# Optimization experiments

Measured on AMD Instinct MI355X. Metric: run time of the kernel, lower is better.

Reference implementation:

```python
import jax, jax.numpy as jnp
import numpy as np

DT = 0.01          # discretization timestep (init kwarg dt)
DAMP_MIN = 5e-4    # minimum damping (init kwarg damp_min)
BATCH, SEQ, D_IN, N_STATE = 16, 2048, 1024, 128


def setup_inputs() -> dict:
    key = jax.random.key(0)
    k1, k2, k3, k4, k5 = jax.random.split(key, 5)
    u = jax.random.normal(k1, (BATCH, SEQ, D_IN), jnp.float32)
    # A_real init: randn*0.1 - damp_min, then clamped to <= -damp_min (stability)
    A_real = jnp.minimum(jax.random.normal(k2, (N_STATE,), jnp.float32) * 0.1 - DAMP_MIN, -DAMP_MIN)
    A_imag = jax.random.normal(k3, (N_STATE,), jnp.float32)
    B = jax.random.normal(k4, (N_STATE, D_IN), jnp.float32) * 0.02
    C = jax.random.normal(k5, (D_IN, N_STATE), jnp.float32) * 0.02
    return {"u": u, "A_real": A_real, "A_imag": A_imag, "B": B, "C": C}


def reference(u, A_real, A_imag, B, C):
    """Real-input path of StableResonantSSM.

    Bilinear discretization of diagonal complex A:
      a_disc = (1 + dt/2 * a) / (1 - dt/2 * a)          (elementwise, A diagonal)
      B_disc = sqrt(dt) * B / (1 - dt/2 * a)            (row-wise scaling)
    Recurrence: h_t = a_disc * h_{t-1} + B_disc @ u_t;  y_t = Re(C @ h_t).
    """
    dt = jnp.float32(DT)
    a = (A_real + 1j * A_imag).astype(jnp.complex64)          # (N,)
    denom = 1.0 - (dt / 2) * a                                 # (N,) complex
    a_disc = (1.0 + (dt / 2) * a) / denom                      # (N,)
    B_disc = (jnp.sqrt(dt) * B.astype(jnp.complex64)) / denom[:, None]  # (N, D)

    # Precompute all input injections as one GEMM: (T, B, N) complex
    Bu = jnp.einsum('btd,nd->tbn', u, B_disc)

    def step(h, bu_t):
        h = a_disc * h + bu_t
        return h, h

    h0 = jnp.zeros((u.shape[0], a.shape[0]), jnp.complex64)
    _, hs = jax.lax.scan(step, h0, Bu)                         # hs: (T, B, N)

    # C is real, so Re(C @ h) == C @ Re(h)
    y = jnp.einsum('tbn,dn->btd', hs.real, C)                  # (B, T, D)
    return y
```

## Files before the change

### kernel.cpp

```cpp
#include <hip/hip_runtime.h>
#include <hip/hip_bf16.h>
#include <cstdint>

#define DT_F    0.01f
#define NB      16
#define T_SEQ   2048
#define DD      1024
#define NS      128
#define CHUNK   64
#define NCH     32

using f32x4  = __attribute__((ext_vector_type(4))) float;
using bf16x8 = __attribute__((ext_vector_type(8))) short;
using fl4    = __attribute__((ext_vector_type(4))) float;

#define AS1(p) ((const __attribute__((address_space(1))) void*)(p))
#define AS3(p) ((__attribute__((address_space(3))) void*)(p))

__device__ __forceinline__ unsigned short f2bf(float f) {
  union { float f; unsigned u; } v; v.f = f;
  unsigned r = v.u + 0x7fffu + ((v.u >> 16) & 1u);
  return (unsigned short)(r >> 16);
}
__device__ __forceinline__ float bf2f(unsigned short s) {
  union { unsigned u; float f; } v; v.u = ((unsigned)s) << 16;
  return v.f;
}
__device__ __forceinline__ unsigned short f2bf_hw(float f) {
  __hip_bfloat16 h = __float2bfloat16(f);
  return __builtin_bit_cast(unsigned short, h);
}

__global__ void prep_all(const float* __restrict__ Ar, const float* __restrict__ Ai,
                         const float* __restrict__ B, const float* __restrict__ C,
                         unsigned short* __restrict__ W, unsigned short* __restrict__ Cb,
                         float* __restrict__ ad) {
  const int blk = blockIdx.x;
  const int tid = threadIdx.x;
  if (blk < 512) {
    const int i = blk * 256 + tid;
    Cb[i] = f2bf(C[i]);
    return;
  }
  const int n = blk - 512;
  const float ar = Ar[n], ai = Ai[n];
  const float dr = 1.f - 0.5f * DT_F * ar;
  const float di = -0.5f * DT_F * ai;
  const float inv = 1.f / (dr * dr + di * di);
  const float nr = 1.f + 0.5f * DT_F * ar;
  const float ni = 0.5f * DT_F * ai;
  if (tid == 0) {
    ad[n]      = (nr * dr + ni * di) * inv;
    ad[NS + n] = (ni * dr - nr * di) * inv;
  }
  const float s  = sqrtf(DT_F);
  const float cr = s * dr * inv;
  const float ci = -s * di * inv;
  for (int d = tid; d < DD; d += 256) {
    const float b = B[(size_t)n * DD + d];
    W[(size_t)n * DD + d]        = f2bf(b * cr);
    W[(size_t)(NS + n) * DD + d] = f2bf(b * ci);
  }
}

__global__ __launch_bounds__(256) void gemm1(const float* __restrict__ U,
                                             const unsigned short* __restrict__ Bw,
                                             unsigned short* __restrict__ Bu) {
  __shared__ __align__(16) unsigned short As[128 * 64];
  __shared__ __align__(16) unsigned short Bs[128 * 64];
  const int tid  = threadIdx.x;
  const int lane = tid & 63;
  const int wave = tid >> 6;

  const int L   = blockIdx.x;
  const int xcd = L & 7;
  const int k   = L >> 3;
  const int bm  = xcd * 32 + (k >> 1);
  const int bn  = k & 1;
  const int rowA0 = bm * 128, colB0 = bn * 128;
  const int wm = (wave >> 1) * 64, wn = (wave & 1) * 64;

  f32x4 acc[4][4];
  const f32x4 zero = {0.f, 0.f, 0.f, 0.f};
#pragma unroll
  for (int i = 0; i < 4; ++i)
#pragma unroll
    for (int j = 0; j < 4; ++j) acc[i][j] = zero;

  const int srow = tid >> 3;
  const int scol = (tid & 7) * 8;
  const int grow = wave * 8 + (lane >> 3);
  const int gcol = (lane & 7) * 8;

  for (int k0 = 0; k0 < DD; k0 += 64) {
    __syncthreads();
#pragma unroll
    for (int it = 0; it < 4; ++it) {
      const unsigned short* gb = Bw + (size_t)(colB0 + it * 32 + grow) * DD + k0 + gcol;
      __builtin_amdgcn_global_load_lds(AS1(gb), AS3(&Bs[(it * 32 + wave * 8) * 64]), 16, 0, 0);
    }
#pragma unroll
    for (int it = 0; it < 4; ++it) {
      const int r = it * 32 + srow;
      const float* ga = U + (size_t)(rowA0 + r) * DD + k0 + scol;
      fl4 v0 = *(const fl4*)ga;
      fl4 v1 = *(const fl4*)(ga + 4);
      bf16x8 pk;
#pragma unroll
      for (int e = 0; e < 4; ++e) { pk[e] = (short)f2bf_hw(v0[e]); pk[4 + e] = (short)f2bf_hw(v1[e]); }
      *(bf16x8*)&As[r * 64 + scol] = pk;
    }
    __syncthreads();
#pragma unroll
    for (int ks = 0; ks < 2; ++ks) {
      bf16x8 af[4], bfr[4];
#pragma unroll
      for (int i = 0; i < 4; ++i)
        af[i] = *(const bf16x8*)&As[(wm + i * 16 + (lane & 15)) * 64 + ks * 32 + (lane >> 4) * 8];
#pragma unroll
      for (int j = 0; j < 4; ++j)
        bfr[j] = *(const bf16x8*)&Bs[(wn + j * 16 + (lane & 15)) * 64 + ks * 32 + (lane >> 4) * 8];
#pragma unroll
      for (int i = 0; i < 4; ++i)
#pragma unroll
        for (int j = 0; j < 4; ++j)
          acc[i][j] = __builtin_amdgcn_mfma_f32_16x16x32_bf16(af[i], bfr[j], acc[i][j], 0, 0, 0);
    }
  }

#pragma unroll
  for (int i = 0; i < 4; ++i) {
    const int r0 = rowA0 + wm + i * 16 + (lane >> 4) * 4;
#pragma unroll
    for (int j = 0; j < 4; ++j) {
      const int c = colB0 + wn + j * 16 + (lane & 15);
#pragma unroll
      for (int q = 0; q < 4; ++q)
        Bu[(size_t)(r0 + q) * 256 + c] = f2bf_hw(acc[i][j][q]);
    }
  }
}

__global__ void scan_finals(const unsigned short* __restrict__ Bu,
                            const float* __restrict__ ad, float* __restrict__ F) {
  const int c = blockIdx.x, b = blockIdx.y;
  const int n = threadIdx.x;
  const float ar = ad[n], ai = ad[NS + n];
  float hr = 0.f, hi = 0.f;
  const unsigned short* p = Bu + ((size_t)b * T_SEQ + (size_t)c * CHUNK) * 256;
#pragma unroll 8
  for (int t = 0; t < CHUNK; ++t) {
    const float br = bf2f(p[t * 256 + n]);
    const float bi = bf2f(p[t * 256 + 128 + n]);
    const float nr = fmaf(ar, hr, fmaf(-ai, hi, br));
    const float ni = fmaf(ar, hi, fmaf(ai, hr, bi));
    hr = nr; hi = ni;
  }
  F[((size_t)b * NCH + c) * 256 + n]       = hr;
  F[((size_t)b * NCH + c) * 256 + 128 + n] = hi;
}

__global__ __launch_bounds__(256) void gemm2s(const unsigned short* __restrict__ Bu,
                                              const float* __restrict__ F,
                                              const float* __restrict__ ad,
                                              const unsigned short* __restrict__ Cb,
                                              float* __restrict__ y) {
  __shared__ __align__(16) unsigned short Hl[64 * 128];
  const int tid  = threadIdx.x;
  const int lane = tid & 63;
  const int wave = tid >> 6;
  const int L = blockIdx.x;
  const int b = L >> 5;
  const int c = L & 31;

  if (tid < 128) {
    const int n = tid;
    const float ar = ad[n], ai = ad[NS + n];
    float alr = ar, ali = ai;
#pragma unroll
    for (int s = 0; s < 6; ++s) {
      const float tr = alr * alr - ali * ali;
      const float ti = 2.f * alr * ali;
      alr = tr; ali = ti;
    }
    float hr = 0.f, hi = 0.f;
    for (int cc = 0; cc < c; ++cc) {
      const float fr = F[((size_t)b * NCH + cc) * 256 + n];
      const float fi = F[((size_t)b * NCH + cc) * 256 + 128 + n];
      const float nr = fmaf(alr, hr, fmaf(-ali, hi, fr));
      const float ni = fmaf(alr, hi, fmaf(ali, hr, fi));
      hr = nr; hi = ni;
    }
    const unsigned short* p = Bu + ((size_t)b * T_SEQ + (size_t)c * CHUNK) * 256;
#pragma unroll 8
    for (int t = 0; t < CHUNK; ++t) {
      const float br = bf2f(p[t * 256 + n]);
      const float bi = bf2f(p[t * 256 + 128 + n]);
      const float nr = fmaf(ar, hr, fmaf(-ai, hi, br));
      const float ni = fmaf(ar, hi, fmaf(ai, hr, bi));
      hr = nr; hi = ni;
      const int byte = t * 256 + ((n * 2) ^ ((t & 7) << 4));
      *(unsigned short*)((char*)Hl + byte) = f2bf(hr);
    }
  }
  __syncthreads();

  const size_t row0 = (size_t)b * T_SEQ + (size_t)c * CHUNK;
#pragma unroll
  for (int cg = 0; cg < 4; ++cg) {
    const int d0 = wave * 256 + cg * 64;
    f32x4 acc[4][4];
    const f32x4 zero = {0.f, 0.f, 0.f, 0.f};
#pragma unroll
    for (int i = 0; i < 4; ++i)
#pragma unroll
      for (int j = 0; j < 4; ++j) acc[i][j] = zero;

#pragma unroll
    for (int ks = 0; ks < 4; ++ks) {
      bf16x8 af[4], bfr[4];
#pragma unroll
      for (int i = 0; i < 4; ++i) {
        const int r = i * 16 + (lane & 15);
        const int byte = r * 256 + ((ks * 64 + (lane >> 4) * 16) ^ ((r & 7) << 4));
        af[i] = *(const bf16x8*)((const char*)Hl + byte);
      }
#pragma unroll
      for (int j = 0; j < 4; ++j) {
        const unsigned short* gb = Cb + (size_t)(d0 + j * 16 + (lane & 15)) * NS + ks * 32 + (lane >> 4) * 8;
        bfr[j] = *(const bf16x8*)gb;
      }
#pragma unroll
      for (int i = 0; i < 4; ++i)
#pragma unroll
        for (int j = 0; j < 4; ++j)
          acc[i][j] = __builtin_amdgcn_mfma_f32_16x16x32_bf16(af[i], bfr[j], acc[i][j], 0, 0, 0);
    }

#pragma unroll
    for (int i = 0; i < 4; ++i) {
      const size_t r0 = row0 + i * 16 + (lane >> 4) * 4;
#pragma unroll
      for (int j = 0; j < 4; ++j) {
        const int d = d0 + j * 16 + (lane & 15);
#pragma unroll
        for (int q = 0; q < 4; ++q)
          y[(r0 + q) * DD + d] = acc[i][j][q];
      }
    }
  }
}

extern "C" void kernel_launch(void* const* d_in, const int* in_sizes, int n_in,
                              void* d_out, int out_size, void* d_ws, size_t ws_size,
                              hipStream_t stream) {
  const float* u  = (const float*)d_in[0];
  const float* Ar = (const float*)d_in[1];
  const float* Ai = (const float*)d_in[2];
  const float* B  = (const float*)d_in[3];
  const float* C  = (const float*)d_in[4];
  float* y = (float*)d_out;
  char* ws = (char*)d_ws;

  unsigned short* W  = (unsigned short*)(ws);
  unsigned short* Cb = (unsigned short*)(ws + (512 << 10));
  float*          ad = (float*)(ws + (768 << 10));
  unsigned short* Bu = (unsigned short*)(ws + (1 << 20));
  float*          F  = (float*)(ws + (1 << 20) + 16777216);

  prep_all<<<dim3(640), dim3(256), 0, stream>>>(Ar, Ai, B, C, W, Cb, ad);
  gemm1<<<dim3(512), dim3(256), 0, stream>>>(u, W, Bu);
  scan_finals<<<dim3(NCH, NB), dim3(128), 0, stream>>>(Bu, ad, F);
  gemm2s<<<dim3(NB * NCH), dim3(256), 0, stream>>>(Bu, F, ad, Cb, y);
}
```

Measured before the change: 89.91 us.

## Fuse input GEMM with chunk-local scan and apply carry correction in output GEMM

The input-projection GEMM now tiles one 64-step chunk by all 256 complex state columns per block, so each block can run the chunk-local scan from LDS right after the MFMA loop. It writes the local states (bf16) and chunk finals, which removes the separate scan_finals kernel and the re-read of Bu. The output kernel loads the local states via global_load_lds, then adds the propagated carry (a^(t+1) times the incoming state) instead of rescanning the chunk. In exchange, the B operand is reloaded per 64-row block, the carry term adds an extra bf16 rounding, and occupancy depends on 40KB of LDS.

```diff
diff --git a/kernel.cpp b/kernel.cpp
--- a/kernel.cpp
+++ b/kernel.cpp
@@ -31,10 +31,19 @@
   return __builtin_bit_cast(unsigned short, h);
 }
 
+__device__ __forceinline__ void adisc(float Arn, float Ain, float& ar, float& ai) {
+  const float dr = 1.f - 0.5f * DT_F * Arn;
+  const float di = -0.5f * DT_F * Ain;
+  const float inv = 1.f / (dr * dr + di * di);
+  const float nr = 1.f + 0.5f * DT_F * Arn;
+  const float nim = 0.5f * DT_F * Ain;
+  ar = (nr * dr + nim * di) * inv;
+  ai = (nim * dr - nr * di) * inv;
+}
+
 __global__ void prep_all(const float* __restrict__ Ar, const float* __restrict__ Ai,
                          const float* __restrict__ B, const float* __restrict__ C,
-                         unsigned short* __restrict__ W, unsigned short* __restrict__ Cb,
-                         float* __restrict__ ad) {
+                         unsigned short* __restrict__ W, unsigned short* __restrict__ Cb) {
   const int blk = blockIdx.x;
   const int tid = threadIdx.x;
   if (blk < 512) {
@@ -47,12 +56,6 @@
   const float dr = 1.f - 0.5f * DT_F * ar;
   const float di = -0.5f * DT_F * ai;
   const float inv = 1.f / (dr * dr + di * di);
-  const float nr = 1.f + 0.5f * DT_F * ar;
-  const float ni = 0.5f * DT_F * ai;
-  if (tid == 0) {
-    ad[n]      = (nr * dr + ni * di) * inv;
-    ad[NS + n] = (ni * dr - nr * di) * inv;
-  }
   const float s  = sqrtf(DT_F);
   const float cr = s * dr * inv;
   const float ci = -s * di * inv;
@@ -63,22 +66,22 @@
   }
 }
 
-__global__ __launch_bounds__(256) void gemm1(const float* __restrict__ U,
-                                             const unsigned short* __restrict__ Bw,
-                                             unsigned short* __restrict__ Bu) {
-  __shared__ __align__(16) unsigned short As[128 * 64];
-  __shared__ __align__(16) unsigned short Bs[128 * 64];
+__global__ __launch_bounds__(256, 2) void gemm1s(const float* __restrict__ U,
+                                                 const float* __restrict__ Ar,
+                                                 const float* __restrict__ Ai,
+                                                 const unsigned short* __restrict__ W,
+                                                 unsigned short* __restrict__ Hs,
+                                                 float* __restrict__ F) {
+  __shared__ __align__(16) char smem[40960];
+  unsigned short* As = (unsigned short*)smem;
+  unsigned short* Bs = (unsigned short*)(smem + 8192);
+  char*           Bt = smem;
+
   const int tid  = threadIdx.x;
   const int lane = tid & 63;
   const int wave = tid >> 6;
-
-  const int L   = blockIdx.x;
-  const int xcd = L & 7;
-  const int k   = L >> 3;
-  const int bm  = xcd * 32 + (k >> 1);
-  const int bn  = k & 1;
-  const int rowA0 = bm * 128, colB0 = bn * 128;
-  const int wm = (wave >> 1) * 64, wn = (wave & 1) * 64;
+  const int blk  = blockIdx.x;
+  const size_t m0 = (size_t)blk * CHUNK;
 
   f32x4 acc[4][4];
   const f32x4 zero = {0.f, 0.f, 0.f, 0.f};
@@ -87,28 +90,33 @@
 #pragma unroll
     for (int j = 0; j < 4; ++j) acc[i][j] = zero;
 
-  const int srow = tid >> 3;
-  const int scol = (tid & 7) * 8;
-  const int grow = wave * 8 + (lane >> 3);
-  const int gcol = (lane & 7) * 8;
+  const int srow  = tid >> 2;
+  const int scol  = (tid & 3) * 16;
+  const int growl = lane >> 3;
+  const int gcol  = (lane & 7) * 8;
 
   for (int k0 = 0; k0 < DD; k0 += 64) {
     __syncthreads();
 #pragma unroll
-    for (int it = 0; it < 4; ++it) {
-      const unsigned short* gb = Bw + (size_t)(colB0 + it * 32 + grow) * DD + k0 + gcol;
-      __builtin_amdgcn_global_load_lds(AS1(gb), AS3(&Bs[(it * 32 + wave * 8) * 64]), 16, 0, 0);
-    }
-#pragma unroll
-    for (int it = 0; it < 4; ++it) {
-      const int r = it * 32 + srow;
-      const float* ga = U + (size_t)(rowA0 + r) * DD + k0 + scol;
+    for (int g = 0; g < 8; ++g) {
+      const int row = wave * 64 + g * 8;
+      const unsigned short* gb = W + (size_t)(row + growl) * DD + k0 + gcol;
+      __builtin_amdgcn_global_load_lds(AS1(gb), AS3(&Bs[row * 64]), 16, 0, 0);
+    }
+    {
+      const float* ga = U + (m0 + srow) * DD + k0 + scol;
       fl4 v0 = *(const fl4*)ga;
       fl4 v1 = *(const fl4*)(ga + 4);
-      bf16x8 pk;
-#pragma unroll
-      for (int e = 0; e < 4; ++e) { pk[e] = (short)f2bf_hw(v0[e]); pk[4 + e] = (short)f2bf_hw(v1[e]); }
-      *(bf16x8*)&As[r * 64 + scol] = pk;
+      fl4 v2 = *(const fl4*)(ga + 8);
+      fl4 v3 = *(const fl4*)(ga + 12);
+      bf16x8 p0, p1;
+#pragma unroll
+      for (int e = 0; e < 4; ++e) {
+        p0[e] = (short)f2bf_hw(v0[e]); p0[4 + e] = (short)f2bf_hw(v1[e]);
+        p1[e] = (short)f2bf_hw(v2[e]); p1[4 + e] = (short)f2bf_hw(v3[e]);
+      }
+      *(bf16x8*)&As[srow * 64 + scol]     = p0;
+      *(bf16x8*)&As[srow * 64 + scol + 8] = p1;
     }
     __syncthreads();
 #pragma unroll
@@ -116,10 +124,10 @@
       bf16x8 af[4], bfr[4];
 #pragma unroll
       for (int i = 0; i < 4; ++i)
-        af[i] = *(const bf16x8*)&As[(wm + i * 16 + (lane & 15)) * 64 + ks * 32 + (lane >> 4) * 8];
+        af[i] = *(const bf16x8*)&As[(i * 16 + (lane & 15)) * 64 + ks * 32 + (lane >> 4) * 8];
 #pragma unroll
       for (int j = 0; j < 4; ++j)
-        bfr[j] = *(const bf16x8*)&Bs[(wn + j * 16 + (lane & 15)) * 64 + ks * 32 + (lane >> 4) * 8];
+        bfr[j] = *(const bf16x8*)&Bs[(wave * 64 + j * 16 + (lane & 15)) * 64 + ks * 32 + (lane >> 4) * 8];
 #pragma unroll
       for (int i = 0; i < 4; ++i)
 #pragma unroll
@@ -127,94 +135,109 @@
           acc[i][j] = __builtin_amdgcn_mfma_f32_16x16x32_bf16(af[i], bfr[j], acc[i][j], 0, 0, 0);
     }
   }
+  __syncthreads();
 
 #pragma unroll
   for (int i = 0; i < 4; ++i) {
-    const int r0 = rowA0 + wm + i * 16 + (lane >> 4) * 4;
 #pragma unroll
     for (int j = 0; j < 4; ++j) {
-      const int c = colB0 + wn + j * 16 + (lane & 15);
-#pragma unroll
-      for (int q = 0; q < 4; ++q)
-        Bu[(size_t)(r0 + q) * 256 + c] = f2bf_hw(acc[i][j][q]);
-    }
-  }
-}
-
-__global__ void scan_finals(const unsigned short* __restrict__ Bu,
-                            const float* __restrict__ ad, float* __restrict__ F) {
-  const int c = blockIdx.x, b = blockIdx.y;
-  const int n = threadIdx.x;
-  const float ar = ad[n], ai = ad[NS + n];
-  float hr = 0.f, hi = 0.f;
-  const unsigned short* p = Bu + ((size_t)b * T_SEQ + (size_t)c * CHUNK) * 256;
+      const int cc = wave * 64 + j * 16 + (lane & 15);
+#pragma unroll
+      for (int q = 0; q < 4; ++q) {
+        const int t = i * 16 + (lane >> 4) * 4 + q;
+        *(unsigned short*)(Bt + t * 512 + ((cc * 2) ^ ((t & 7) << 4))) = f2bf_hw(acc[i][j][q]);
+      }
+    }
+  }
+  __syncthreads();
+
+  if (tid < 128) {
+    const int n = tid;
+    float ar, ai; adisc(Ar[n], Ai[n], ar, ai);
+    float hr = 0.f, hi = 0.f;
+    unsigned short* o = Hs + (size_t)blk * (CHUNK * NS) + n;
 #pragma unroll 8
-  for (int t = 0; t < CHUNK; ++t) {
-    const float br = bf2f(p[t * 256 + n]);
-    const float bi = bf2f(p[t * 256 + 128 + n]);
-    const float nr = fmaf(ar, hr, fmaf(-ai, hi, br));
-    const float ni = fmaf(ar, hi, fmaf(ai, hr, bi));
-    hr = nr; hi = ni;
-  }
-  F[((size_t)b * NCH + c) * 256 + n]       = hr;
-  F[((size_t)b * NCH + c) * 256 + 128 + n] = hi;
-}
-
-__global__ __launch_bounds__(256) void gemm2s(const unsigned short* __restrict__ Bu,
-                                              const float* __restrict__ F,
-                                              const float* __restrict__ ad,
-                                              const unsigned short* __restrict__ Cb,
-                                              float* __restrict__ y) {
-  __shared__ __align__(16) unsigned short Hl[64 * 128];
+    for (int t = 0; t < CHUNK; ++t) {
+      const int reByte = t * 512 + ((n * 2) ^ ((t & 7) << 4));
+      const float br = bf2f(*(const unsigned short*)(Bt + reByte));
+      const float bi = bf2f(*(const unsigned short*)(Bt + reByte + 256));
+      const float xr = fmaf(ar, hr, fmaf(-ai, hi, br));
+      const float xi = fmaf(ar, hi, fmaf(ai, hr, bi));
+      hr = xr; hi = xi;
+      o[t * NS] = f2bf(hr);
+    }
+    F[(size_t)blk * 256 + n]       = hr;
+    F[(size_t)blk * 256 + 128 + n] = hi;
+  }
+}
+
+__global__ __launch_bounds__(256, 2) void gemm2s(const unsigned short* __restrict__ Hs,
+                                                 const float* __restrict__ F,
+                                                 const float* __restrict__ Ar,
+                                                 const float* __restrict__ Ai,
+                                                 const unsigned short* __restrict__ Cb,
+                                                 float* __restrict__ y) {
+  __shared__ __align__(16) char Hl[64 * 256];
   const int tid  = threadIdx.x;
   const int lane = tid & 63;
   const int wave = tid >> 6;
-  const int L = blockIdx.x;
-  const int b = L >> 5;
-  const int c = L & 31;
+  const int blk  = blockIdx.x;
+  const int c    = blk & 31;
+  const size_t m0 = (size_t)blk * CHUNK;
+
+  const char* tile = (const char*)Hs + (size_t)blk * (CHUNK * NS * 2);
+#pragma unroll
+  for (int g = 0; g < 4; ++g) {
+    const int r0 = wave * 16 + g * 4;
+    const int r  = r0 + (lane >> 4);
+    const int srcOff = r * 256 + ((((lane & 15)) * 16) ^ ((r & 7) << 4));
+    __builtin_amdgcn_global_load_lds(AS1(tile + srcOff), AS3(Hl + r0 * 256), 16, 0, 0);
+  }
+  __syncthreads();
 
   if (tid < 128) {
     const int n = tid;
-    const float ar = ad[n], ai = ad[NS + n];
-    float alr = ar, ali = ai;
-#pragma unroll
-    for (int s = 0; s < 6; ++s) {
-      const float tr = alr * alr - ali * ali;
-      const float ti = 2.f * alr * ali;
-      alr = tr; ali = ti;
-    }
-    float hr = 0.f, hi = 0.f;
-    for (int cc = 0; cc < c; ++cc) {
-      const float fr = F[((size_t)b * NCH + cc) * 256 + n];
-      const float fi = F[((size_t)b * NCH + cc) * 256 + 128 + n];
-      const float nr = fmaf(alr, hr, fmaf(-ali, hi, fr));
-      const float ni = fmaf(alr, hi, fmaf(ali, hr, fi));
-      hr = nr; hi = ni;
-    }
-    const unsigned short* p = Bu + ((size_t)b * T_SEQ + (size_t)c * CHUNK) * 256;
+    float ar, ai; adisc(Ar[n], Ai[n], ar, ai);
+    if (c != 0) {
+      float alr = ar, ali = ai;
+#pragma unroll
+      for (int s = 0; s < 6; ++s) {
+        const float tr = alr * alr - ali * ali;
+        const float ti = 2.f * alr * ali;
+        alr = tr; ali = ti;
+      }
+      float cr = 0.f, ci = 0.f;
+      const float* Fb = F + (size_t)(blk - c) * 256;
+      for (int cc = 0; cc < c; ++cc) {
+        const float fr = Fb[(size_t)cc * 256 + n];
+        const float fi = Fb[(size_t)cc * 256 + 128 + n];
+        const float xr = fmaf(alr, cr, fmaf(-ali, ci, fr));
+        const float xi = fmaf(alr, ci, fmaf(ali, cr, fi));
+        cr = xr; ci = xi;
+      }
+      float gr = ar * cr - ai * ci;
+      float gi = ar * ci + ai * cr;
 #pragma unroll 8
-    for (int t = 0; t < CHUNK; ++t) {
-      const float br = bf2f(p[t * 256 + n]);
-      const float bi = bf2f(p[t * 256 + 128 + n]);
-      const float nr = fmaf(ar, hr, fmaf(-ai, hi, br));
-      const float ni = fmaf(ar, hi, fmaf(ai, hr, bi));
-      hr = nr; hi = ni;
-      const int byte = t * 256 + ((n * 2) ^ ((t & 7) << 4));
-      *(unsigned short*)((char*)Hl + byte) = f2bf(hr);
-    }
-  }
-  __syncthreads();
-
-  const size_t row0 = (size_t)b * T_SEQ + (size_t)c * CHUNK;
+      for (int t = 0; t < CHUNK; ++t) {
+        unsigned short* pp = (unsigned short*)(Hl + t * 256 + ((n * 2) ^ ((t & 7) << 4)));
+        *pp = f2bf(bf2f(*pp) + gr);
+        const float xr = ar * gr - ai * gi;
+        const float xi = ar * gi + ai * gr;
+        gr = xr; gi = xi;
+      }
+    }
+  }
+  __syncthreads();
+
+  const f32x4 zero = {0.f, 0.f, 0.f, 0.f};
 #pragma unroll
   for (int cg = 0; cg < 4; ++cg) {
     const int d0 = wave * 256 + cg * 64;
-    f32x4 acc[4][4];
-    const f32x4 zero = {0.f, 0.f, 0.f, 0.f};
+    f32x4 oacc[4][4];
 #pragma unroll
     for (int i = 0; i < 4; ++i)
 #pragma unroll
-      for (int j = 0; j < 4; ++j) acc[i][j] = zero;
+      for (int j = 0; j < 4; ++j) oacc[i][j] = zero;
 
 #pragma unroll
     for (int ks = 0; ks < 4; ++ks) {
@@ -222,30 +245,26 @@
 #pragma unroll
       for (int i = 0; i < 4; ++i) {
         const int r = i * 16 + (lane & 15);
-        const int byte = r * 256 + ((ks * 64 + (lane >> 4) * 16) ^ ((r & 7) << 4));
-        af[i] = *(const bf16x8*)((const char*)Hl + byte);
-      }
-#pragma unroll
-      for (int j = 0; j < 4; ++j) {
-        const unsigned short* gb = Cb + (size_t)(d0 + j * 16 + (lane & 15)) * NS + ks * 32 + (lane >> 4) * 8;
-        bfr[j] = *(const bf16x8*)gb;
-      }
+        af[i] = *(const bf16x8*)(Hl + r * 256 + ((ks * 64 + (lane >> 4) * 16) ^ ((r & 7) << 4)));
+      }
+#pragma unroll
+      for (int j = 0; j < 4; ++j)
+        bfr[j] = *(const bf16x8*)(Cb + (size_t)(d0 + j * 16 + (lane & 15)) * NS + ks * 32 + (lane >> 4) * 8);
 #pragma unroll
       for (int i = 0; i < 4; ++i)
 #pragma unroll
         for (int j = 0; j < 4; ++j)
-          acc[i][j] = __builtin_amdgcn_mfma_f32_16x16x32_bf16(af[i], bfr[j], acc[i][j], 0, 0, 0);
-    }
-
+          oacc[i][j] = __builtin_amdgcn_mfma_f32_16x16x32_bf16(af[i], bfr[j], oacc[i][j], 0, 0, 0);
+    }
 #pragma unroll
     for (int i = 0; i < 4; ++i) {
-      const size_t r0 = row0 + i * 16 + (lane >> 4) * 4;
+      const size_t r0 = m0 + i * 16 + (lane >> 4) * 4;
 #pragma unroll
       for (int j = 0; j < 4; ++j) {
         const int d = d0 + j * 16 + (lane & 15);
 #pragma unroll
         for (int q = 0; q < 4; ++q)
-          y[(r0 + q) * DD + d] = acc[i][j][q];
+          y[(r0 + q) * DD + d] = oacc[i][j][q];
       }
     }
   }
@@ -264,12 +283,10 @@
 
   unsigned short* W  = (unsigned short*)(ws);
   unsigned short* Cb = (unsigned short*)(ws + (512 << 10));
-  float*          ad = (float*)(ws + (768 << 10));
-  unsigned short* Bu = (unsigned short*)(ws + (1 << 20));
-  float*          F  = (float*)(ws + (1 << 20) + 16777216);
-
-  prep_all<<<dim3(640), dim3(256), 0, stream>>>(Ar, Ai, B, C, W, Cb, ad);
-  gemm1<<<dim3(512), dim3(256), 0, stream>>>(u, W, Bu);
-  scan_finals<<<dim3(NCH, NB), dim3(128), 0, stream>>>(Bu, ad, F);
-  gemm2s<<<dim3(NB * NCH), dim3(256), 0, stream>>>(Bu, F, ad, Cb, y);
-}
+  float*          F  = (float*)(ws + (768 << 10));
+  unsigned short* Hs = (unsigned short*)(ws + (1280 << 10));
+
+  prep_all<<<dim3(640), dim3(256), 0, stream>>>(Ar, Ai, B, C, W, Cb);
+  gemm1s<<<dim3(NB * NCH), dim3(256), 0, stream>>>(u, Ar, Ai, W, Hs, F);
+  gemm2s<<<dim3(NB * NCH), dim3(256), 0, stream>>>(Hs, F, Ar, Ai, Cb, y);
+}
```

Measured after the change: 84.02 us. 6.6% less time.
